# Optimization experiments

Hardware: AMD Instinct MI355X
Metric: run time of the kernel (lower is better)

Reference implementation:

```python
import jax, jax.numpy as jnp
import numpy as np

N_EXPERT = 8
TOP_K = 2
NEG_INF = -1e9  # finite sentinel so softmax grads stay well-defined


def setup_inputs() -> dict:
    key = jax.random.key(0)
    ks = jax.random.split(key, 8)
    B, S, D, F, E = 2, 2048, 1024, 4096, N_EXPERT
    sd = 1.0 / np.sqrt(D)
    sf = 1.0 / np.sqrt(F)
    return {
        "x": jax.random.normal(ks[0], (B, S, D), jnp.float32),
        "noise": jax.random.normal(ks[1], (B, S, E), jnp.float32),
        "Wr": jax.random.normal(ks[2], (D, E), jnp.float32) * sd,
        "br": jnp.zeros((E,), jnp.float32),
        "Wn": jax.random.normal(ks[3], (D, E), jnp.float32) * sd,
        "bn": jnp.zeros((E,), jnp.float32),
        "W1": jax.random.normal(ks[4], (E, D, F), jnp.float32) * sd,
        "b1": jnp.zeros((E, F), jnp.float32),
        "W2": jax.random.normal(ks[5], (E, F, D), jnp.float32) * sf,
        "b2": jnp.zeros((E, D), jnp.float32),
    }


def reference(x, noise, Wr, br, Wn, bn, W1, b1, W2, b2):
    # NoisyTopkRouter: logits + noise * softplus(noise_logits)
    logits = jnp.einsum("bsd,de->bse", x, Wr) + br
    noise_logits = jnp.einsum("bsd,de->bse", x, Wn) + bn
    noisy = logits + noise * jax.nn.softplus(noise_logits)

    # keep only top-k logits, -inf elsewhere, softmax over experts
    _, top_ids = jax.lax.top_k(noisy, TOP_K)                  # [B,S,K]
    sel = jnp.sum(jax.nn.one_hot(top_ids, N_EXPERT, dtype=noisy.dtype), axis=-2) > 0  # [B,S,E]
    gates = jax.nn.softmax(jnp.where(sel, noisy, NEG_INF), axis=-1)  # zeros off top-k

    # Expert MLP: Linear -> ReLU -> Linear (dropout = 0 at inference).
    # Gates are exactly zero for non-selected experts, so the dense einsum
    # combine equals the original masked gather/scatter-add.
    h = jax.nn.relu(jnp.einsum("bsd,edf->ebsf", x, W1) + b1[:, None, None, :])
    eo = jnp.einsum("ebsf,efd->ebsd", h, W2) + b2[:, None, None, :]
    return jnp.einsum("bse,ebsd->bsd", gates, eo)
```

## Files before the change

### kernel.cpp

```cpp
#include <hip/hip_runtime.h>

#define T_TOK 4096
#define DDIM 1024
#define FDIM 4096
#define NE 8
#define NPAIR 8192
#define MAXT128 72

typedef short bf16x8 __attribute__((ext_vector_type(8)));
typedef float f32x4 __attribute__((ext_vector_type(4)));

__device__ inline unsigned short f2bf(float f) {
  union { float f; unsigned u; } a; a.f = f;
  unsigned r = a.u + 0x7fffu + ((a.u >> 16) & 1u);
  return (unsigned short)(r >> 16);
}

__device__ __forceinline__ void gload16(const void* g, void* l) {
  __builtin_amdgcn_global_load_lds(
      (const __attribute__((address_space(1))) unsigned int*)g,
      (__attribute__((address_space(3))) unsigned int*)l, 16, 0, 0);
}

__global__ __launch_bounds__(256) void router_kernel(
    const float* __restrict__ x, const float* __restrict__ noise,
    const float* __restrict__ Wr, const float* __restrict__ br,
    const float* __restrict__ Wn, const float* __restrict__ bn,
    int* __restrict__ tok_top, float* __restrict__ tok_gate,
    ushort* __restrict__ xb)
{
  int t = blockIdx.x * 4 + (threadIdx.x >> 6);
  int lane = threadIdx.x & 63;
  const float* xr = x + (size_t)t * DDIM;
  ushort* xo = xb + (size_t)t * DDIM;
  float accR[NE] = {}, accN[NE] = {};
  for (int d = lane; d < DDIM; d += 64) {
    float xv = xr[d];
    xo[d] = f2bf(xv);
    const float* wr = Wr + (size_t)d * NE;
    const float* wn = Wn + (size_t)d * NE;
#pragma unroll
    for (int e = 0; e < NE; ++e) {
      accR[e] = fmaf(xv, wr[e], accR[e]);
      accN[e] = fmaf(xv, wn[e], accN[e]);
    }
  }
#pragma unroll
  for (int off = 32; off > 0; off >>= 1) {
#pragma unroll
    for (int e = 0; e < NE; ++e) {
      accR[e] += __shfl_xor(accR[e], off);
      accN[e] += __shfl_xor(accN[e], off);
    }
  }
  if (lane == 0) {
    float noisy[NE];
#pragma unroll
    for (int e = 0; e < NE; ++e) {
      float lg = accR[e] + br[e];
      float nl = accN[e] + bn[e];
      float sp = fmaxf(nl, 0.f) + log1pf(expf(-fabsf(nl)));
      noisy[e] = lg + noise[(size_t)t * NE + e] * sp;
    }
    int e0 = 0;
#pragma unroll
    for (int e = 1; e < NE; ++e) if (noisy[e] > noisy[e0]) e0 = e;
    int e1 = (e0 == 0) ? 1 : 0;
#pragma unroll
    for (int e = 0; e < NE; ++e)
      if (e != e0 && e != e1 && noisy[e] > noisy[e1]) e1 = e;
    float v0 = noisy[e0], v1 = noisy[e1];
    float ex = __expf(v1 - v0);
    float inv = 1.f / (1.f + ex);
    tok_top[t * 2] = e0; tok_top[t * 2 + 1] = e1;
    tok_gate[t * 2] = inv; tok_gate[t * 2 + 1] = ex * inv;
  }
}

__global__ __launch_bounds__(256) void scan_scatter_kernel(
    const int* __restrict__ tok_top, int* __restrict__ off, int* __restrict__ tiles,
    int* __restrict__ pair_tok, int* __restrict__ tok_ppos)
{
  __shared__ int smat[NE][256];
  __shared__ int tot[NE];
  __shared__ int loff[NE];
  int tid = threadIdx.x;
  int c[NE] = {};
  for (int i = 0; i < 16; ++i) {
    int t = tid * 16 + i;
    int e0 = tok_top[2 * t], e1 = tok_top[2 * t + 1];
#pragma unroll
    for (int e = 0; e < NE; ++e) c[e] += (e0 == e) + (e1 == e);
  }
#pragma unroll
  for (int e = 0; e < NE; ++e) smat[e][tid] = c[e];
  __syncthreads();
  if (tid < NE) {
    int s = 0;
    for (int j = 0; j < 256; ++j) { int v = smat[tid][j]; smat[tid][j] = s; s += v; }
    tot[tid] = s;
  }
  __syncthreads();
  if (tid == 0) {
    int s = 0, nt = 0;
    for (int e = 0; e < NE; ++e) {
      loff[e] = s; off[e] = s;
      int tt = (tot[e] + 127) >> 7;
      for (int m = 0; m < tt; ++m) tiles[1 + nt++] = (e << 8) | m;
      s += tot[e];
    }
    off[NE] = s;
    tiles[0] = nt;
  }
  __syncthreads();
  for (int i = 0; i < 16; ++i) {
    int t = tid * 16 + i;
#pragma unroll
    for (int k = 0; k < 2; ++k) {
      int e = tok_top[2 * t + k];
      int pos = loff[e] + smat[e][tid];
      smat[e][tid] = smat[e][tid] + 1;
      pair_tok[pos] = t;
      tok_ppos[2 * t + k] = pos;
    }
  }
}

__global__ __launch_bounds__(256) void transpose_bf_kernel(
    const float* __restrict__ W1, const float* __restrict__ W2,
    ushort* __restrict__ WT1, ushort* __restrict__ WT2)
{
  __shared__ float tile[64][65];
  int z = blockIdx.z;
  const float* src; ushort* dst; int R, C, bx, by;
  if (z < NE) {
    src = W1 + (size_t)z * DDIM * FDIM; dst = WT1 + (size_t)z * FDIM * DDIM;
    R = DDIM; C = FDIM; bx = blockIdx.x; by = blockIdx.y;
  } else {
    src = W2 + (size_t)(z - NE) * FDIM * DDIM; dst = WT2 + (size_t)(z - NE) * DDIM * FDIM;
    R = FDIM; C = DDIM; bx = blockIdx.y; by = blockIdx.x;
  }
  int c0 = bx * 64, r0 = by * 64;
  int tid = threadIdx.x;
  int tr = tid >> 4;
  int tc4 = (tid & 15) * 4;
#pragma unroll
  for (int i = 0; i < 64; i += 16) {
    float4 v = *(const float4*)(src + (size_t)(r0 + tr + i) * C + c0 + tc4);
    tile[tr + i][tc4] = v.x; tile[tr + i][tc4 + 1] = v.y;
    tile[tr + i][tc4 + 2] = v.z; tile[tr + i][tc4 + 3] = v.w;
  }
  __syncthreads();
  int cc = tid >> 4;
  int rr4 = (tid & 15) * 4;
#pragma unroll
  for (int i = 0; i < 64; i += 16) {
    int c = cc + i;
    ushort4 o;
    o.x = f2bf(tile[rr4][c]); o.y = f2bf(tile[rr4 + 1][c]);
    o.z = f2bf(tile[rr4 + 2][c]); o.w = f2bf(tile[rr4 + 3][c]);
    *(ushort4*)(dst + (size_t)(c0 + c) * R + r0 + rr4) = o;
  }
}

template<int KD, int ND, int EPI, int INDIR>
__global__ __launch_bounds__(256) void gemm4_kernel(
    const ushort* __restrict__ A, const ushort* __restrict__ BT,
    const int* __restrict__ off, const int* __restrict__ tiles,
    const int* __restrict__ pair_tok, const float* __restrict__ bias,
    ushort* __restrict__ Hout, float* __restrict__ EOout)
{
  constexpr int GX = ND / 128;
  constexpr int NKT = KD / 64;
  __shared__ __align__(16) char lds[2 * 32768];

  int total = tiles[0] * GX;
  int orig = blockIdx.x + GX * (int)blockIdx.y;
  if (orig >= total) return;
  int q = total >> 3, r = total & 7, xcd = orig & 7, idx = orig >> 3;
  int wg = (xcd < r ? xcd * (q + 1) : r * (q + 1) + (xcd - r) * q) + idx;
  int ti = wg / GX, bx = wg - ti * GX;

  int te = tiles[1 + ti];
  int e = te >> 8, mt = te & 255;
  int base = off[e];
  int cnt = off[e + 1] - base;
  int m0 = mt << 7, n0 = bx << 7;

  int tid = threadIdx.x, lane = tid & 63, wid = tid >> 6;
  int wr = wid >> 1, wc = wid & 1;

  const char* aptr[4];
  const char* bptr[4];
  {
    const char* Ab = (const char*)A;
    const char* Bgb = (const char*)(BT + ((size_t)e * ND + n0) * KD);
#pragma unroll
    for (int c = 0; c < 4; ++c) {
      int ch = c * 256 + tid;
      int row = ch >> 3, b = (ch & 7) * 16;
      int bsw = b ^ ((row & 7) << 4);
      int mr = m0 + row; if (mr >= cnt) mr = cnt - 1;
      int ar = INDIR ? pair_tok[base + mr] : base + mr;
      aptr[c] = Ab + (size_t)ar * (KD * 2) + bsw;
      bptr[c] = Bgb + (size_t)row * (KD * 2) + bsw;
    }
  }

  auto STAGE = [&](int bufi) {
    char* d = lds + bufi * 32768;
#pragma unroll
    for (int c = 0; c < 4; ++c) {
      int ch = c * 256 + tid;
      gload16(aptr[c], d + ch * 16);
      gload16(bptr[c], d + 16384 + ch * 16);
      aptr[c] += 128;
      bptr[c] += 128;
    }
  };

  int lr = lane & 15, hi = lane >> 4;
  int swl = (lane & 7) << 4;
  int offA[2], offB[2];
#pragma unroll
  for (int ks = 0; ks < 2; ++ks) {
    int kk = (ks * 64 + hi * 16) ^ swl;
    offA[ks] = (wr * 64 + lr) * 128 + kk;
    offB[ks] = (wc * 64 + lr) * 128 + kk;
  }

  f32x4 acc[4][4] = {};

  STAGE(0);
  asm volatile("s_waitcnt vmcnt(0)" ::: "memory");
  __builtin_amdgcn_sched_barrier(0);
  __builtin_amdgcn_s_barrier();

  for (int t = 0; t < NKT; ++t) {
    if (t + 1 < NKT) STAGE((t + 1) & 1);

    const char* pa = lds + (t & 1) * 32768;
    const char* pb = pa + 16384;
    bf16x8 af[4][2], bv[4][2];
#pragma unroll
    for (int m = 0; m < 4; ++m)
#pragma unroll
      for (int ks = 0; ks < 2; ++ks)
        af[m][ks] = *(const bf16x8*)(pa + offA[ks] + m * 2048);
#pragma unroll
    for (int n = 0; n < 4; ++n)
#pragma unroll
      for (int ks = 0; ks < 2; ++ks)
        bv[n][ks] = *(const bf16x8*)(pb + offB[ks] + n * 2048);
#pragma unroll
    for (int ks = 0; ks < 2; ++ks)
#pragma unroll
      for (int m = 0; m < 4; ++m)
#pragma unroll
        for (int n = 0; n < 4; ++n)
          acc[m][n] = __builtin_amdgcn_mfma_f32_16x16x32_bf16(
              af[m][ks], bv[n][ks], acc[m][n], 0, 0, 0);

    asm volatile("s_waitcnt lgkmcnt(0)" ::: "memory");
    if (t + 1 < NKT) asm volatile("s_waitcnt vmcnt(0)" ::: "memory");
    __builtin_amdgcn_sched_barrier(0);
    __builtin_amdgcn_s_barrier();
  }

  float bvv[4];
#pragma unroll
  for (int n = 0; n < 4; ++n)
    bvv[n] = bias[(size_t)e * ND + n0 + wc * 64 + n * 16 + lr];
  int rq = hi << 2;
#pragma unroll
  for (int m = 0; m < 4; ++m) {
#pragma unroll
    for (int qq = 0; qq < 4; ++qq) {
      int rr = m0 + wr * 64 + m * 16 + rq + qq;
      if (rr < cnt) {
#pragma unroll
        for (int n = 0; n < 4; ++n) {
          int col = n0 + wc * 64 + n * 16 + lr;
          float v = acc[m][n][qq] + bvv[n];
          if (EPI == 0) {
            v = fmaxf(v, 0.f);
            Hout[(size_t)(base + rr) * ND + col] = f2bf(v);
          } else {
            EOout[(size_t)(base + rr) * ND + col] = v;
          }
        }
      }
    }
  }
}

__global__ __launch_bounds__(256) void combine_kernel(
    const float* __restrict__ eo, const int* __restrict__ tok_ppos,
    const float* __restrict__ tok_gate, float* __restrict__ out)
{
  int t = blockIdx.x;
  int tid = threadIdx.x;
  int p0 = tok_ppos[t * 2], p1 = tok_ppos[t * 2 + 1];
  float g0 = tok_gate[t * 2], g1 = tok_gate[t * 2 + 1];
  float4 a = ((const float4*)(eo + (size_t)p0 * DDIM))[tid];
  float4 b = ((const float4*)(eo + (size_t)p1 * DDIM))[tid];
  float4 o;
  o.x = g0 * a.x + g1 * b.x;
  o.y = g0 * a.y + g1 * b.y;
  o.z = g0 * a.z + g1 * b.z;
  o.w = g0 * a.w + g1 * b.w;
  ((float4*)(out + (size_t)t * DDIM))[tid] = o;
}

extern "C" void kernel_launch(void* const* d_in, const int* in_sizes, int n_in,
                              void* d_out, int out_size, void* d_ws, size_t ws_size,
                              hipStream_t stream)
{
  const float* x     = (const float*)d_in[0];
  const float* noise = (const float*)d_in[1];
  const float* Wr    = (const float*)d_in[2];
  const float* br    = (const float*)d_in[3];
  const float* Wn    = (const float*)d_in[4];
  const float* bn    = (const float*)d_in[5];
  const float* W1    = (const float*)d_in[6];
  const float* b1    = (const float*)d_in[7];
  const float* W2    = (const float*)d_in[8];
  const float* b2    = (const float*)d_in[9];
  float* out = (float*)d_out;

  char* ws = (char*)d_ws;
  size_t o = 0;
  auto alloc = [&](size_t sz) {
    void* p = ws + o;
    o = (o + sz + 255) & ~(size_t)255;
    return p;
  };
  ushort* WT1 = (ushort*)alloc((size_t)NE * FDIM * DDIM * 2);
  ushort* WT2 = (ushort*)alloc((size_t)NE * DDIM * FDIM * 2);
  ushort* XB  = (ushort*)alloc((size_t)T_TOK * DDIM * 2);
  ushort* H   = (ushort*)alloc((size_t)(NPAIR + 256) * FDIM * 2);
  float*  EO  = (float*)alloc((size_t)(NPAIR + 256) * DDIM * 4);
  int*    TOK_TOP  = (int*)alloc(T_TOK * 2 * 4);
  float*  TOK_GATE = (float*)alloc(T_TOK * 2 * 4);
  int*    TOK_PPOS = (int*)alloc(T_TOK * 2 * 4);
  int*    PAIR_TOK = (int*)alloc((NPAIR + 256) * 4);
  int*    OFF = (int*)alloc(64);
  int*    TILES = (int*)alloc((1 + MAXT128) * 4);

  router_kernel<<<T_TOK / 4, 256, 0, stream>>>(x, noise, Wr, br, Wn, bn,
                                               TOK_TOP, TOK_GATE, XB);
  scan_scatter_kernel<<<1, 256, 0, stream>>>(TOK_TOP, OFF, TILES, PAIR_TOK, TOK_PPOS);
  transpose_bf_kernel<<<dim3(64, 16, 16), 256, 0, stream>>>(W1, W2, WT1, WT2);
  gemm4_kernel<DDIM, FDIM, 0, 1>
      <<<dim3(FDIM / 128, MAXT128), 256, 0, stream>>>(XB, WT1, OFF, TILES, PAIR_TOK, b1, H, nullptr);
  gemm4_kernel<FDIM, DDIM, 1, 0>
      <<<dim3(DDIM / 128, MAXT128), 256, 0, stream>>>(H, WT2, OFF, TILES, PAIR_TOK, b2, nullptr, EO);
  combine_kernel<<<T_TOK, 256, 0, stream>>>(EO, TOK_PPOS, TOK_GATE, out);
}
```

Measured before the change: 359.6 us.

## Single-buffer GEMM LDS and raise occupancy to four blocks per CU

Replaces the double-buffered LDS prefetch pipeline with a single 32 KB buffer loaded and consumed each k-step between two __syncthreads. It also adds a min-blocks-per-CU hint of 4 to launch bounds. The aim is to let more workgroups reside per CU, hiding global load latency across blocks instead of within one block. The cost is that global loads no longer overlap with MFMA work inside a block, and the hint may cap registers for the 64-float accumulator.

```diff
diff --git a/kernel.cpp b/kernel.cpp
--- a/kernel.cpp
+++ b/kernel.cpp
@@ -164,7 +164,7 @@
 }
 
 template<int KD, int ND, int EPI, int INDIR>
-__global__ __launch_bounds__(256) void gemm4_kernel(
+__global__ __launch_bounds__(256, 4) void gemm4_kernel(
     const ushort* __restrict__ A, const ushort* __restrict__ BT,
     const int* __restrict__ off, const int* __restrict__ tiles,
     const int* __restrict__ pair_tok, const float* __restrict__ bias,
@@ -172,7 +172,7 @@
 {
   constexpr int GX = ND / 128;
   constexpr int NKT = KD / 64;
-  __shared__ __align__(16) char lds[2 * 32768];
+  __shared__ __align__(16) char lds[32768];
 
   int total = tiles[0] * GX;
   int orig = blockIdx.x + GX * (int)blockIdx.y;
@@ -207,51 +207,38 @@
     }
   }
 
-  auto STAGE = [&](int bufi) {
-    char* d = lds + bufi * 32768;
+  int lr = lane & 15, hi = lane >> 4;
+  int swl = (lane & 7) << 4;
+  int aBase0 = (wr * 64 + lr) * 128 + ((hi * 16) ^ swl);
+  int aBase1 = (wr * 64 + lr) * 128 + ((64 + hi * 16) ^ swl);
+  int bBase0 = 16384 + (wc * 64 + lr) * 128 + ((hi * 16) ^ swl);
+  int bBase1 = 16384 + (wc * 64 + lr) * 128 + ((64 + hi * 16) ^ swl);
+
+  f32x4 acc[4][4] = {};
+
+  for (int t = 0; t < NKT; ++t) {
+    __syncthreads();
 #pragma unroll
     for (int c = 0; c < 4; ++c) {
       int ch = c * 256 + tid;
-      gload16(aptr[c], d + ch * 16);
-      gload16(bptr[c], d + 16384 + ch * 16);
+      gload16(aptr[c], lds + ch * 16);
+      gload16(bptr[c], lds + 16384 + ch * 16);
       aptr[c] += 128;
       bptr[c] += 128;
     }
-  };
-
-  int lr = lane & 15, hi = lane >> 4;
-  int swl = (lane & 7) << 4;
-  int offA[2], offB[2];
-#pragma unroll
-  for (int ks = 0; ks < 2; ++ks) {
-    int kk = (ks * 64 + hi * 16) ^ swl;
-    offA[ks] = (wr * 64 + lr) * 128 + kk;
-    offB[ks] = (wc * 64 + lr) * 128 + kk;
-  }
-
-  f32x4 acc[4][4] = {};
-
-  STAGE(0);
-  asm volatile("s_waitcnt vmcnt(0)" ::: "memory");
-  __builtin_amdgcn_sched_barrier(0);
-  __builtin_amdgcn_s_barrier();
-
-  for (int t = 0; t < NKT; ++t) {
-    if (t + 1 < NKT) STAGE((t + 1) & 1);
-
-    const char* pa = lds + (t & 1) * 32768;
-    const char* pb = pa + 16384;
+    __syncthreads();
+
     bf16x8 af[4][2], bv[4][2];
 #pragma unroll
-    for (int m = 0; m < 4; ++m)
-#pragma unroll
-      for (int ks = 0; ks < 2; ++ks)
-        af[m][ks] = *(const bf16x8*)(pa + offA[ks] + m * 2048);
-#pragma unroll
-    for (int n = 0; n < 4; ++n)
-#pragma unroll
-      for (int ks = 0; ks < 2; ++ks)
-        bv[n][ks] = *(const bf16x8*)(pb + offB[ks] + n * 2048);
+    for (int m = 0; m < 4; ++m) {
+      af[m][0] = *(const bf16x8*)(lds + aBase0 + m * 2048);
+      af[m][1] = *(const bf16x8*)(lds + aBase1 + m * 2048);
+    }
+#pragma unroll
+    for (int n = 0; n < 4; ++n) {
+      bv[n][0] = *(const bf16x8*)(lds + bBase0 + n * 2048);
+      bv[n][1] = *(const bf16x8*)(lds + bBase1 + n * 2048);
+    }
 #pragma unroll
     for (int ks = 0; ks < 2; ++ks)
 #pragma unroll
@@ -260,11 +247,6 @@
         for (int n = 0; n < 4; ++n)
           acc[m][n] = __builtin_amdgcn_mfma_f32_16x16x32_bf16(
               af[m][ks], bv[n][ks], acc[m][n], 0, 0, 0);
-
-    asm volatile("s_waitcnt lgkmcnt(0)" ::: "memory");
-    if (t + 1 < NKT) asm volatile("s_waitcnt vmcnt(0)" ::: "memory");
-    __builtin_amdgcn_sched_barrier(0);
-    __builtin_amdgcn_s_barrier();
   }
 
   float bvv[4];
```

New measurement: 432.3 us. 1.2x slower.
